# Kernel tuning notes

Measured on AMD Instinct MI355X. Metric: run time of the kernel, lower is better.

Reference implementation:

```python
import jax, jax.numpy as jnp
import numpy as np

DIM = 2048
N_HEADS = 16
HEAD_DIM = DIM // N_HEADS
ROPE_DIMS = 16
SEQ_LEN = 512
BATCH = 16


def _rope_cache(T):
    # freqs: [T, rd/2]
    inv = 1.0 / (10000.0 ** (jnp.arange(0, ROPE_DIMS, 2, dtype=jnp.float32) / ROPE_DIMS))
    t = jnp.arange(T, dtype=jnp.float32)
    freqs = jnp.outer(t, inv)
    return jnp.cos(freqs), jnp.sin(freqs)


def _apply_rope(x, cos, sin):
    # x: [B, H, T, hd]; rotate first ROPE_DIMS dims (half-split style)
    rd = ROPE_DIMS
    x_rope, x_pass = x[..., :rd], x[..., rd:]
    x1, x2 = x_rope[..., : rd // 2], x_rope[..., rd // 2:]
    c = cos[None, None, :, :]
    s = sin[None, None, :, :]
    rot = jnp.concatenate([x1 * c - x2 * s, x2 * c + x1 * s], axis=-1)
    return jnp.concatenate([rot, x_pass], axis=-1)


def setup_inputs() -> dict:
    key = jax.random.key(0)
    k1, k2, k3 = jax.random.split(key, 3)
    x = jax.random.normal(k1, (BATCH, SEQ_LEN, DIM), dtype=jnp.float32)
    Wqkv = jax.random.normal(k2, (DIM, 3 * DIM), dtype=jnp.float32) * (1.0 / np.sqrt(DIM))
    Wout = jax.random.normal(k3, (DIM, DIM), dtype=jnp.float32) * (1.0 / np.sqrt(DIM))
    return {"x": x, "Wqkv": Wqkv, "Wout": Wout}


def reference(x, Wqkv, Wout):
    B, T, C = x.shape
    H, hd = N_HEADS, HEAD_DIM
    qkv = (x @ Wqkv).reshape(B, T, 3, H, hd)
    q, k, v = qkv[:, :, 0], qkv[:, :, 1], qkv[:, :, 2]  # [B, T, H, hd]
    q = jnp.transpose(q, (0, 2, 1, 3))  # [B, H, T, hd]
    k = jnp.transpose(k, (0, 2, 1, 3))
    v = jnp.transpose(v, (0, 2, 1, 3))
    cos, sin = _rope_cache(T)
    q = _apply_rope(q, cos, sin)
    k = _apply_rope(k, cos, sin)
    scale = 1.0 / np.sqrt(hd)
    scores = jnp.einsum('bhqd,bhkd->bhqk', q, k) * scale
    causal = jnp.tril(jnp.ones((T, T), dtype=bool))
    scores = jnp.where(causal[None, None], scores, jnp.finfo(scores.dtype).min)
    attn = jax.nn.softmax(scores, axis=-1)
    y = jnp.einsum('bhqk,bhkd->bhqd', attn, v)  # [B, H, T, hd]
    y = jnp.transpose(y, (0, 2, 1, 3)).reshape(B, T, C)
    return y @ Wout
```

## Files before the change

### kernel.cpp

```cpp
#include <hip/hip_runtime.h>
#include <hip/hip_bf16.h>
#include <math.h>

using bf16 = __hip_bfloat16;
typedef short s16x8 __attribute__((ext_vector_type(8)));
typedef short s16x4 __attribute__((ext_vector_type(4)));
typedef float f32x4 __attribute__((ext_vector_type(4)));

#define DIM_C   2048
#define NHEADS  16
#define HEADD   128
#define SEQT    512
#define NBATCH  16
#define MROWS   (NBATCH*SEQT)
#define QKVN    (3*DIM_C)
#define QKN     (2*DIM_C)

static __device__ __forceinline__ float bf2f(bf16 v){ return __bfloat162float(v); }

static __device__ __forceinline__ void gl16(const void* g, void* l){
    __builtin_amdgcn_global_load_lds(
        reinterpret_cast<__attribute__((address_space(1))) void*>(
            (unsigned long long)g),
        reinterpret_cast<__attribute__((address_space(3))) void*>(
            (unsigned long long)l),
        16, 0, 0);
}

__global__ void k_cvt(const float* __restrict__ in, bf16* __restrict__ out, int n){
    size_t i = ((size_t)blockIdx.x*blockDim.x + threadIdx.x)*8;
    if (i >= (size_t)n) return;
    float4 a = *(const float4*)(in+i);
    float4 b = *(const float4*)(in+i+4);
    union { bf16 o[8]; s16x8 v; } u;
    u.o[0]=__float2bfloat16(a.x); u.o[1]=__float2bfloat16(a.y);
    u.o[2]=__float2bfloat16(a.z); u.o[3]=__float2bfloat16(a.w);
    u.o[4]=__float2bfloat16(b.x); u.o[5]=__float2bfloat16(b.y);
    u.o[6]=__float2bfloat16(b.z); u.o[7]=__float2bfloat16(b.w);
    *(s16x8*)(out+i) = u.v;
}

__global__ void k_transpose_cvt(const float* __restrict__ in, bf16* __restrict__ out,
                                int R, int C){
    __shared__ float tile[32][33];
    int c0 = blockIdx.x*32, r0 = blockIdx.y*32;
    int tx = threadIdx.x, ty = threadIdx.y;
    #pragma unroll
    for(int i=0;i<4;i++)
        tile[ty+8*i][tx] = in[(size_t)(r0+ty+8*i)*C + c0+tx];
    __syncthreads();
    #pragma unroll
    for(int i=0;i<4;i++)
        out[(size_t)(c0+ty+8*i)*R + r0+tx] = __float2bfloat16(tile[tx][ty+8*i]);
}

static __device__ __forceinline__ void store_c(bf16* p, float v){ *p = __float2bfloat16(v); }
static __device__ __forceinline__ void store_c(float* p, float v){ *p = v; }

#define BAR()   __builtin_amdgcn_s_barrier()
#define SCHED() __builtin_amdgcn_sched_barrier(0)
#define LGKM0() asm volatile("s_waitcnt lgkmcnt(0)" ::: "memory")
#define VM6()   asm volatile("s_waitcnt vmcnt(6)"   ::: "memory")
#define VM0()   asm volatile("s_waitcnt vmcnt(0)"   ::: "memory")

template<typename OutT, int MODE>
__global__ __launch_bounds__(512, 2) void k_gemm256(const bf16* __restrict__ A,
                                                    const bf16* __restrict__ Bt,
                                                    OutT* __restrict__ C,
                                                    bf16* __restrict__ vt,
                                                    int M, int N, int K){
    __shared__ __align__(16) bf16 AS[2][2][128*64];
    __shared__ __align__(16) bf16 BS[2][2][128*64];
    const int tid = threadIdx.x;
    const int wave = tid>>6, lane = tid&63, quad = lane>>4, l16 = lane&15;
    const int wm = wave>>2, wn = wave&3;

    const int nbx = gridDim.x;
    const int nwg = gridDim.x*gridDim.y;
    int bid = blockIdx.y*nbx + blockIdx.x;
    int swz = (bid&7)*(nwg>>3) + (bid>>3);
    int by = swz / nbx, bx = swz - by*nbx;
    const size_t rowbase = (size_t)by * 256;
    const size_t colbase = (size_t)bx * 256;
    const int NT = K>>6;

    f32x4 acc[8][4];
    #pragma unroll
    for(int i=0;i<8;i++)
        #pragma unroll
        for(int j=0;j<4;j++) acc[i][j] = (f32x4)(0.f);

    int cb0 = wave*64,        cc0 = cb0 + lane;
    int cb1 = 512 + wave*64,  cc1 = cb1 + lane;
    int ri0 = cc0>>3, gg0 = (cc0&7)^(ri0&7);
    int ri1 = cc1>>3, gg1 = (cc1&7)^(ri1&7);
    const bf16* pA0[2];  const bf16* pA1[2];
    const bf16* pB0[2];  const bf16* pB1[2];
    pA0[0] = A  + (rowbase + (size_t)(((ri0>>6)<<7) + (ri0&63)))*(size_t)K + gg0*8;
    pA0[1] = A  + (rowbase + (size_t)(((ri1>>6)<<7) + (ri1&63)))*(size_t)K + gg1*8;
    pA1[0] = pA0[0] + (size_t)64*K;  pA1[1] = pA0[1] + (size_t)64*K;
    pB0[0] = Bt + (colbase + (size_t)(((ri0>>5)<<6) + (ri0&31)))*(size_t)K + gg0*8;
    pB0[1] = Bt + (colbase + (size_t)(((ri1>>5)<<6) + (ri1&31)))*(size_t)K + gg1*8;
    pB1[0] = pB0[0] + (size_t)32*K;  pB1[1] = pB0[1] + (size_t)32*K;
    const int dE0 = cb0*8, dE1 = cb1*8;

    const int x7 = l16 & 7;
    int aB[2], bB[2];
    #pragma unroll
    for(int kc=0;kc<2;kc++){
        int ch = ((kc*4+quad) ^ x7) << 3;
        aB[kc] = (wm*64 + l16)*64 + ch;
        bB[kc] = (wn*32 + l16)*64 + ch;
    }

    s16x8 af[4][2], bf0[2][2], bf1[2][2];

#define READ_AF(BUF,MH) do{ _Pragma("unroll")                                    \
    for(int kc_=0;kc_<2;kc_++){ _Pragma("unroll")                                \
        for(int mi_=0;mi_<4;mi_++)                                               \
            af[mi_][kc_] = *(const s16x8*)(&AS[BUF][MH][aB[kc_] + mi_*1024]); } }while(0)
#define READ_BF(BUF,NH,DST) do{ _Pragma("unroll")                                \
    for(int kc_=0;kc_<2;kc_++){ _Pragma("unroll")                                \
        for(int nj_=0;nj_<2;nj_++)                                               \
            DST[nj_][kc_] = *(const s16x8*)(&BS[BUF][NH][bB[kc_] + nj_*1024]); } }while(0)
#define MFMA16(BFR,MH,NH) do{ _Pragma("unroll")                                  \
    for(int kc_=0;kc_<2;kc_++){ _Pragma("unroll")                                \
        for(int mi_=0;mi_<4;mi_++){ _Pragma("unroll")                            \
            for(int nj_=0;nj_<2;nj_++)                                           \
                acc[(MH)*4+mi_][(NH)*2+nj_] =                                    \
                    __builtin_amdgcn_mfma_f32_16x16x32_bf16(                     \
                        af[mi_][kc_], BFR[nj_][kc_],                             \
                        acc[(MH)*4+mi_][(NH)*2+nj_], 0,0,0); } } }while(0)

#define STG_A0(BUF,OFF) do{ gl16(pA0[0]+(OFF), &AS[BUF][0][dE0]);                \
                            gl16(pA0[1]+(OFF), &AS[BUF][0][dE1]); }while(0)
#define STG_A1(BUF,OFF) do{ gl16(pA1[0]+(OFF), &AS[BUF][1][dE0]);                \
                            gl16(pA1[1]+(OFF), &AS[BUF][1][dE1]); }while(0)
#define STG_B0(BUF,OFF) do{ gl16(pB0[0]+(OFF), &BS[BUF][0][dE0]);                \
                            gl16(pB0[1]+(OFF), &BS[BUF][0][dE1]); }while(0)
#define STG_B1(BUF,OFF) do{ gl16(pB1[0]+(OFF), &BS[BUF][1][dE0]);                \
                            gl16(pB1[1]+(OFF), &BS[BUF][1][dE1]); }while(0)

#define TILE(BUF,O1,O2,GA1,GR)                                                   \
    do{                                                                          \
                                                                         \
        if (GA1) STG_A1(BUF^1, O1);                                              \
        READ_AF(BUF,0); READ_BF(BUF,0,bf0);                                      \
        BAR(); LGKM0(); SCHED();                                                 \
        __builtin_amdgcn_s_setprio(1);  MFMA16(bf0,0,0);                         \
        __builtin_amdgcn_s_setprio(0);                                           \
        BAR(); SCHED();                                                          \
                                                                         \
        if (GR) STG_A0(BUF,O2);                                                  \
        READ_BF(BUF,1,bf1);                                                      \
        BAR(); LGKM0(); SCHED();                                                 \
        __builtin_amdgcn_s_setprio(1);  MFMA16(bf1,0,1);                         \
        __builtin_amdgcn_s_setprio(0);                                           \
        BAR(); SCHED();                                                          \
                                                                         \
        if (GR) STG_B0(BUF,O2);                                                  \
        READ_AF(BUF,1);                                                          \
        BAR(); LGKM0(); SCHED();                                                 \
        __builtin_amdgcn_s_setprio(1);  MFMA16(bf0,1,0);                         \
        __builtin_amdgcn_s_setprio(0);                                           \
        BAR(); SCHED();                                                          \
                                                                         \
        if (GR){ STG_B1(BUF,O2); VM6(); } else { VM0(); }                        \
        BAR(); SCHED();                                                          \
        __builtin_amdgcn_s_setprio(1);  MFMA16(bf1,1,1);                         \
        __builtin_amdgcn_s_setprio(0);                                           \
        BAR(); SCHED();                                                          \
    }while(0)

    STG_A0(0,0); STG_B0(0,0); STG_B1(0,0); STG_A1(0,0);
    STG_A0(1,64); STG_B0(1,64); STG_B1(1,64);
    VM6();
    BAR(); SCHED();

    for(int g=0; g<NT; g+=2){
        const bool p2 = (g+2 < NT), p3 = (g+3 < NT);
        TILE(0, 64, 128, true, p2);
        TILE(1, 128, 192, p2, p3);
        pA0[0]+=128; pA0[1]+=128; pA1[0]+=128; pA1[1]+=128;
        pB0[0]+=128; pB0[1]+=128; pB1[0]+=128; pB1[1]+=128;
    }
#undef TILE
#undef STG_A0
#undef STG_A1
#undef STG_B0
#undef STG_B1
#undef MFMA16
#undef READ_BF
#undef READ_AF

    if (MODE == 0){
        #pragma unroll
        for(int mf=0;mf<8;mf++)
            #pragma unroll
            for(int nf=0;nf<4;nf++)
                #pragma unroll
                for(int r=0;r<4;r++){
                    size_t row = rowbase + wm*128 + mf*16 + quad*4 + r;
                    size_t col = colbase + wn*64  + nf*16 + l16;
                    store_c(C + row*(size_t)N + col, acc[mf][nf][r]);
                }
    } else if (colbase < 4096){
        const bool ropeW = ((wn&1) == 0);
        const float inv = powf(10000.f, -(float)(l16&7)/8.f);
        const bool hi = (l16 >= 8);
        #pragma unroll
        for(int mf=0;mf<8;mf++)
            #pragma unroll
            for(int nf=0;nf<4;nf++)
                #pragma unroll
                for(int r=0;r<4;r++){
                    size_t row = rowbase + wm*128 + mf*16 + quad*4 + r;
                    size_t col = colbase + wn*64  + nf*16 + l16;
                    float val = acc[mf][nf][r];
                    if (nf == 0 && ropeW){
                        int t = (int)(row & 511);
                        float fr = (float)t * inv;
                        float cc = cosf(fr), ss = sinf(fr);
                        float p  = __shfl_xor(val, 8, 64);
                        val = hi ? (val*cc + p*ss) : (val*cc - p*ss);
                    }
                    *( (bf16*)C + row*(size_t)QKN + col ) = __float2bfloat16(val);
                }
    } else {
        #pragma unroll
        for(int nf=0;nf<4;nf++){
            int col = (int)colbase + wn*64 + nf*16 + l16;
            int h   = (col - 4096) >> 7;
            int d   = col & 127;
            #pragma unroll
            for(int mf=0;mf<8;mf++){
                int row0 = (int)rowbase + wm*128 + mf*16 + quad*4;
                int b = row0 >> 9, t0 = row0 & 511;
                union { s16x4 v; bf16 hh[4]; } o;
                #pragma unroll
                for(int r=0;r<4;r++) o.hh[r] = __float2bfloat16(acc[mf][nf][r]);
                *(s16x4*)(vt + ((size_t)((b<<4)+h)*128 + d)*512 + t0) = o.v;
            }
        }
    }
}

__global__ __launch_bounds__(256, 4) void k_attn(const bf16* __restrict__ qk,
                                                 const bf16* __restrict__ vt,
                                                 bf16* __restrict__ y){
    __shared__ __align__(16) bf16 Ks[64*128];
    __shared__ __align__(16) bf16 Vs[128*64];
    __shared__ __align__(16) bf16 Ps[64*64];
    const int id = blockIdx.x;
    const int x  = id & 7, g = id >> 3;
    const int qt = 7 - (g >> 5);
    const int bh = ((g & 31) << 3) | x;
    const int b = bh >> 4, h = bh & 15;
    const int tid = threadIdx.x, wave = tid>>6, lane = tid&63, quad = lane>>4, l16 = lane&15;
    const int qbase = qt*64;
    const size_t rs = QKN;
    const bf16* Qg = qk + ((size_t)b*SEQT)*rs + (size_t)h*HEADD;
    const bf16* Kg = Qg + DIM_C;
    const bf16* Vtbh = vt + ((size_t)bh*HEADD)*SEQT;

    s16x8 qf[4];
    const int qrow = qbase + wave*16 + l16;
    {
        #pragma unroll
        for(int kc=0;kc<4;kc++)
            qf[kc] = *(const s16x8*)(Qg + (size_t)qrow*rs + kc*32 + quad*8);
    }
    f32x4 acc_o[8];
    #pragma unroll
    for(int dt=0;dt<8;dt++) acc_o[dt] = (f32x4)(0.f);
    float lsum = 0.f;
    const float C2 = 0.12751745f;
    const int nkt = qt + 1;

    for(int kt=0; kt<nkt; kt++){
        const int kbase = kt*64;
        const bool diag = (kt == nkt-1);
        __syncthreads();
        #pragma unroll
        for(int i=0;i<4;i++){
            int base = wave*256 + i*64;
            int cc   = base + lane;
            int rk   = cc>>4, gk = (cc&15) ^ (rk&7);
            gl16(Kg + (size_t)(kbase+rk)*rs + gk*8, &Ks[base*8]);
            int rv   = cc>>3, gv = (cc&7) ^ (rv&7);
            gl16(Vtbh + (size_t)rv*SEQT + kbase + gv*8, &Vs[base*8]);
        }
        __syncthreads();
        f32x4 sacc[4];
        #pragma unroll
        for(int ni=0;ni<4;ni++) sacc[ni] = (f32x4)(0.f);
        #pragma unroll
        for(int kc=0;kc<4;kc++){
            const int ch = kc*4 + quad;
            #pragma unroll
            for(int ni=0;ni<4;ni++){
                int r = ni*16 + l16;
                s16x8 kf = *(const s16x8*)(&Ks[r*128 + ((ch ^ (r&7))*8)]);
                sacc[ni] = __builtin_amdgcn_mfma_f32_16x16x32_bf16(kf, qf[kc], sacc[ni], 0,0,0);
            }
        }
        {
            const int row = wave*16 + l16;
            const int r7  = row & 7;
            #pragma unroll
            for(int ni=0;ni<4;ni++){
                union { s16x4 v; bf16 hh[4]; } pk;
                #pragma unroll
                for(int rr=0;rr<4;rr++){
                    float e = exp2f(sacc[ni][rr]*C2);
                    if (diag){ int kcol = kbase + ni*16 + quad*4 + rr; if (kcol > qrow) e = 0.f; }
                    lsum += e;
                    pk.hh[rr] = __float2bfloat16(e);
                }
                int c = ni*2 + (quad>>1);
                *(s16x4*)(&Ps[row*64 + ((c ^ r7)<<3) + ((quad&1)<<2)]) = pk.v;
            }
        }
        #pragma unroll
        for(int kk=0;kk<2;kk++){
            int rw = wave*16 + l16;
            int c  = kk*4 + quad;
            s16x8 pf = *(const s16x8*)(&Ps[rw*64 + ((c ^ (rw&7))<<3)]);
            #pragma unroll
            for(int dt=0;dt<8;dt++){
                int r = dt*16 + l16;
                s16x8 vf = *(const s16x8*)(&Vs[r*64 + ((c ^ (r&7))<<3)]);
                acc_o[dt] = __builtin_amdgcn_mfma_f32_16x16x32_bf16(vf, pf, acc_o[dt], 0,0,0);
            }
        }
    }
    lsum += __shfl_xor(lsum, 16, 64);
    lsum += __shfl_xor(lsum, 32, 64);
    float inv_l = 1.f/lsum;
    size_t base = ((size_t)(b*SEQT) + qrow)*DIM_C + (size_t)h*HEADD;
    #pragma unroll
    for(int dt=0;dt<8;dt++){
        union { s16x4 v; bf16 hh[4]; } o;
        #pragma unroll
        for(int rr=0;rr<4;rr++) o.hh[rr] = __float2bfloat16(acc_o[dt][rr]*inv_l);
        *(s16x4*)(y + base + dt*16 + quad*4) = o.v;
    }
}

extern "C" void kernel_launch(void* const* d_in, const int* in_sizes, int n_in,
                              void* d_out, int out_size, void* d_ws, size_t ws_size,
                              hipStream_t stream){
    const float* x    = (const float*)d_in[0];
    const float* Wqkv = (const float*)d_in[1];
    const float* Wout = (const float*)d_in[2];
    float* out = (float*)d_out;
    char* ws = (char*)d_ws;
    bf16* xb    = (bf16*)(ws + 0);
    bf16* wqkvT = (bf16*)(ws + 33554432);
    bf16* woutT = (bf16*)(ws + 58720256);
    bf16* qkb   = (bf16*)(ws + 67108864);
    bf16* vt    = (bf16*)(ws + 134217728);
    bf16* yb    = (bf16*)(ws + 167772160);

    k_cvt<<<dim3(MROWS*DIM_C/8/256), 256, 0, stream>>>(x, xb, MROWS*DIM_C);
    dim3 tb(32,8);
    k_transpose_cvt<<<dim3(QKVN/32, DIM_C/32), tb, 0, stream>>>(Wqkv, wqkvT, DIM_C, QKVN);
    k_transpose_cvt<<<dim3(DIM_C/32, DIM_C/32), tb, 0, stream>>>(Wout, woutT, DIM_C, DIM_C);

    k_gemm256<bf16,1><<<dim3(QKVN/256, MROWS/256), 512, 0, stream>>>(
        xb, wqkvT, qkb, vt, MROWS, QKVN, DIM_C);
    k_attn<<<dim3(SEQT/64 * NHEADS * NBATCH), 256, 0, stream>>>(qkb, vt, yb);
    k_gemm256<float,0><<<dim3(DIM_C/256, MROWS/256), 512, 0, stream>>>(
        yb, woutT, out, (bf16*)nullptr, MROWS, DIM_C, DIM_C);
}
```

Before: 509.7 us.

## Pipeline K/V staging in attention and move V transpose to separate kernel

The attention loop now prefetches the next K tile while softmax runs and the next V tile after the PV MFMAs. Partial vmcnt waits, barriers and s_setprio around the MFMA blocks are meant to overlap global-to-LDS loads with compute. Separately, the QKV GEMM epilogue now writes V row-major, and a new tiled transpose kernel builds the transposed V layout. This replaces the strided scattered 4-element stores with an extra launch and an extra read/write pass over V. The y buffer now reuses the V scratch region.

After: 499.0 us. 1.02x faster.

```diff
diff --git a/kernel.cpp b/kernel.cpp
--- a/kernel.cpp
+++ b/kernel.cpp
@@ -54,6 +54,22 @@
         out[(size_t)(c0+ty+8*i)*R + r0+tx] = __float2bfloat16(tile[tx][ty+8*i]);
 }
 
+__global__ void k_vtrans(const bf16* __restrict__ vbuf, bf16* __restrict__ vt){
+    __shared__ bf16 tile[32][33];
+    int t0 = blockIdx.x*32, d0 = blockIdx.y*32, bh = blockIdx.z;
+    int b = bh>>4, h = bh&15;
+    int tx = threadIdx.x, ty = threadIdx.y;
+    const bf16* src = vbuf + ((size_t)b*SEQT)*DIM_C + (size_t)h*HEADD;
+    #pragma unroll
+    for(int i=0;i<4;i++)
+        tile[ty+8*i][tx] = src[(size_t)(t0+ty+8*i)*DIM_C + d0+tx];
+    __syncthreads();
+    bf16* dst = vt + ((size_t)bh*HEADD)*SEQT;
+    #pragma unroll
+    for(int i=0;i<4;i++)
+        dst[(size_t)(d0+ty+8*i)*SEQT + t0+tx] = tile[tx][ty+8*i];
+}
+
 static __device__ __forceinline__ void store_c(bf16* p, float v){ *p = __float2bfloat16(v); }
 static __device__ __forceinline__ void store_c(float* p, float v){ *p = v; }
 
@@ -61,13 +77,14 @@
 #define SCHED() __builtin_amdgcn_sched_barrier(0)
 #define LGKM0() asm volatile("s_waitcnt lgkmcnt(0)" ::: "memory")
 #define VM6()   asm volatile("s_waitcnt vmcnt(6)"   ::: "memory")
+#define VM4()   asm volatile("s_waitcnt vmcnt(4)"   ::: "memory")
 #define VM0()   asm volatile("s_waitcnt vmcnt(0)"   ::: "memory")
 
 template<typename OutT, int MODE>
 __global__ __launch_bounds__(512, 2) void k_gemm256(const bf16* __restrict__ A,
                                                     const bf16* __restrict__ Bt,
                                                     OutT* __restrict__ C,
-                                                    bf16* __restrict__ vt,
+                                                    bf16* __restrict__ vbuf,
                                                     int M, int N, int K){
     __shared__ __align__(16) bf16 AS[2][2][128*64];
     __shared__ __align__(16) bf16 BS[2][2][128*64];
@@ -228,20 +245,15 @@
                 }
     } else {
         #pragma unroll
-        for(int nf=0;nf<4;nf++){
-            int col = (int)colbase + wn*64 + nf*16 + l16;
-            int h   = (col - 4096) >> 7;
-            int d   = col & 127;
-            #pragma unroll
-            for(int mf=0;mf<8;mf++){
-                int row0 = (int)rowbase + wm*128 + mf*16 + quad*4;
-                int b = row0 >> 9, t0 = row0 & 511;
-                union { s16x4 v; bf16 hh[4]; } o;
+        for(int mf=0;mf<8;mf++)
+            #pragma unroll
+            for(int nf=0;nf<4;nf++)
                 #pragma unroll
-                for(int r=0;r<4;r++) o.hh[r] = __float2bfloat16(acc[mf][nf][r]);
-                *(s16x4*)(vt + ((size_t)((b<<4)+h)*128 + d)*512 + t0) = o.v;
-            }
-        }
+                for(int r=0;r<4;r++){
+                    size_t row = rowbase + wm*128 + mf*16 + quad*4 + r;
+                    size_t col = colbase + wn*64  + nf*16 + l16 - 4096;
+                    vbuf[row*(size_t)DIM_C + col] = __float2bfloat16(acc[mf][nf][r]);
+                }
     }
 }
 
@@ -277,23 +289,36 @@
     const float C2 = 0.12751745f;
     const int nkt = qt + 1;
 
-    for(int kt=0; kt<nkt; kt++){
-        const int kbase = kt*64;
-        const bool diag = (kt == nkt-1);
-        __syncthreads();
+    auto stageK = [&](int kb){
         #pragma unroll
         for(int i=0;i<4;i++){
             int base = wave*256 + i*64;
             int cc   = base + lane;
             int rk   = cc>>4, gk = (cc&15) ^ (rk&7);
-            gl16(Kg + (size_t)(kbase+rk)*rs + gk*8, &Ks[base*8]);
+            gl16(Kg + (size_t)(kb+rk)*rs + gk*8, &Ks[base*8]);
+        }
+    };
+    auto stageV = [&](int kb){
+        #pragma unroll
+        for(int i=0;i<4;i++){
+            int base = wave*256 + i*64;
+            int cc   = base + lane;
             int rv   = cc>>3, gv = (cc&7) ^ (rv&7);
-            gl16(Vtbh + (size_t)rv*SEQT + kbase + gv*8, &Vs[base*8]);
+            gl16(Vtbh + (size_t)rv*SEQT + kb + gv*8, &Vs[base*8]);
         }
-        __syncthreads();
+    };
+
+    stageK(0); stageV(0);
+
+    for(int kt=0; kt<nkt; kt++){
+        const int kbase = kt*64;
+        const bool diag = (kt == nkt-1);
+        const bool more = (kt+1 < nkt);
+        VM4(); BAR(); SCHED();
         f32x4 sacc[4];
         #pragma unroll
         for(int ni=0;ni<4;ni++) sacc[ni] = (f32x4)(0.f);
+        __builtin_amdgcn_s_setprio(1);
         #pragma unroll
         for(int kc=0;kc<4;kc++){
             const int ch = kc*4 + quad;
@@ -304,6 +329,9 @@
                 sacc[ni] = __builtin_amdgcn_mfma_f32_16x16x32_bf16(kf, qf[kc], sacc[ni], 0,0,0);
             }
         }
+        __builtin_amdgcn_s_setprio(0);
+        SCHED(); BAR(); SCHED();
+        if (more) stageK(kbase+64);
         {
             const int row = wave*16 + l16;
             const int r7  = row & 7;
@@ -321,6 +349,9 @@
                 *(s16x4*)(&Ps[row*64 + ((c ^ r7)<<3) + ((quad&1)<<2)]) = pk.v;
             }
         }
+        if (more){ VM4(); } else { VM0(); }
+        BAR(); SCHED();
+        __builtin_amdgcn_s_setprio(1);
         #pragma unroll
         for(int kk=0;kk<2;kk++){
             int rw = wave*16 + l16;
@@ -333,6 +364,9 @@
                 acc_o[dt] = __builtin_amdgcn_mfma_f32_16x16x32_bf16(vf, pf, acc_o[dt], 0,0,0);
             }
         }
+        __builtin_amdgcn_s_setprio(0);
+        SCHED(); BAR(); SCHED();
+        if (more) stageV(kbase+64);
     }
     lsum += __shfl_xor(lsum, 16, 64);
     lsum += __shfl_xor(lsum, 32, 64);
@@ -359,8 +393,9 @@
     bf16* wqkvT = (bf16*)(ws + 33554432);
     bf16* woutT = (bf16*)(ws + 58720256);
     bf16* qkb   = (bf16*)(ws + 67108864);
-    bf16* vt    = (bf16*)(ws + 134217728);
-    bf16* yb    = (bf16*)(ws + 167772160);
+    bf16* vbuf  = (bf16*)(ws + 134217728);
+    bf16* vt    = (bf16*)(ws + 167772160);
+    bf16* yb    = (bf16*)(ws + 134217728);
 
     k_cvt<<<dim3(MROWS*DIM_C/8/256), 256, 0, stream>>>(x, xb, MROWS*DIM_C);
     dim3 tb(32,8);
@@ -368,7 +403,8 @@
     k_transpose_cvt<<<dim3(DIM_C/32, DIM_C/32), tb, 0, stream>>>(Wout, woutT, DIM_C, DIM_C);
 
     k_gemm256<bf16,1><<<dim3(QKVN/256, MROWS/256), 512, 0, stream>>>(
-        xb, wqkvT, qkb, vt, MROWS, QKVN, DIM_C);
+        xb, wqkvT, qkb, vbuf, MROWS, QKVN, DIM_C);
+    k_vtrans<<<dim3(SEQT/32, HEADD/32, NBATCH*NHEADS), tb, 0, stream>>>(vbuf, vt);
     k_attn<<<dim3(SEQT/64 * NHEADS * NBATCH), 256, 0, stream>>>(qkb, vt, yb);
     k_gemm256<float,0><<<dim3(DIM_C/256, MROWS/256), 512, 0, stream>>>(
         yb, woutT, out, (bf16*)nullptr, MROWS, DIM_C, DIM_C);
```
